# Kernel tuning notes

Hardware: AMD Instinct MI355X
Metric: run time of the kernel (lower is better)

## Reference

```python
import jax, jax.numpy as jnp
import numpy as np

B, N, DIM, HID, MAXN = 2048, 65536, 256, 512, 64
MID_KEY = (MAXN + HID) // 2   # 288
MID_VAL = (DIM + HID) // 2    # 384
MID_DEC = (HID + DIM) // 2    # 384
MID_SZ  = (HID + 1) // 2      # 256

def _ln(x, g, b):
    m = x.mean(-1, keepdims=True)
    v = ((x - m) ** 2).mean(-1, keepdims=True)
    return (x - m) * jax.lax.rsqrt(v + 1e-5) * g + b

def _mish(x):
    return x * jnp.tanh(jax.nn.softplus(x))

def _mlp_ln(x, W1, b1, g, be, W2, b2):
    return _mish(_ln(x @ W1 + b1, g, be)) @ W2 + b2

def _mlp(x, W1, b1, W2, b2):
    return _mish(x @ W1 + b1) @ W2 + b2

def setup_inputs():
    key = jax.random.key(0)
    ks = iter(jax.random.split(key, 40))
    def rn(shape, s=0.05):
        return jax.random.normal(next(ks), shape, jnp.float32) * s
    x = jax.random.normal(next(ks), (N, DIM), jnp.float32)
    batch = jnp.sort(jax.random.randint(next(ks), (N,), 0, B)).astype(jnp.int32)
    z32 = lambda *s: jnp.zeros(s, jnp.float32)
    o32 = lambda *s: jnp.ones(s, jnp.float32)
    return dict(
        x=x, batch=batch, n_batches=B,
        e_rank_W=rn((DIM, 1)), e_rank_b=z32(1),
        e_card_W=rn((1, HID)), e_card_b=z32(HID),
        e_key_W1=rn((MAXN, MID_KEY)), e_key_b1=z32(MID_KEY), e_key_g=o32(MID_KEY), e_key_be=z32(MID_KEY),
        e_key_W2=rn((MID_KEY, HID)), e_key_b2=z32(HID),
        e_val_W1=rn((DIM, MID_VAL)), e_val_b1=z32(MID_VAL), e_val_g=o32(MID_VAL), e_val_be=z32(MID_VAL),
        e_val_W2=rn((MID_VAL, HID)), e_val_b2=z32(HID),
        d_key_W1=rn((MAXN, MID_KEY)), d_key_b1=z32(MID_KEY), d_key_g=o32(MID_KEY), d_key_be=z32(MID_KEY),
        d_key_W2=rn((MID_KEY, HID)), d_key_b2=z32(HID),
        d_dec_W1=rn((HID, MID_DEC)), d_dec_b1=z32(MID_DEC),
        d_dec_W2=rn((MID_DEC, DIM)), d_dec_b2=z32(DIM),
        d_size_W1=rn((HID, MID_SZ)), d_size_b1=z32(MID_SZ), d_size_g=o32(MID_SZ), d_size_be=z32(MID_SZ),
        d_size_W2=rn((MID_SZ, 1)), d_size_b2=z32(1),
    )

def reference(x, batch, n_batches, e_rank_W, e_rank_b, e_card_W, e_card_b,
              e_key_W1, e_key_b1, e_key_g, e_key_be, e_key_W2, e_key_b2,
              e_val_W1, e_val_b1, e_val_g, e_val_be, e_val_W2, e_val_b2,
              d_key_W1, d_key_b1, d_key_g, d_key_be, d_key_W2, d_key_b2,
              d_dec_W1, d_dec_b1, d_dec_W2, d_dec_b2,
              d_size_W1, d_size_b1, d_size_g, d_size_be, d_size_W2, d_size_b2):
    max_n = e_key_W1.shape[0]
    n_pts = x.shape[0]
    # ---- Encoder ----
    n = jax.ops.segment_sum(jnp.ones(n_pts, jnp.float32), batch, num_segments=n_batches).astype(jnp.int32)
    mag = jnp.abs(x @ e_rank_W + e_rank_b)[:, 0]                 # [N]
    sort_key = batch.astype(jnp.float32) * jnp.max(mag) + mag    # sort within each set by |rank|
    idx = jnp.argsort(sort_key)
    xs = x[idx]
    starts = jnp.cumsum(n) - n                                   # per-set offsets (batch is sorted)
    pos_idx = jnp.arange(n_pts) - starts[batch]                  # rank within each set
    pos = jax.nn.one_hot(pos_idx, max_n, dtype=x.dtype)
    y = _mlp_ln(xs, e_val_W1, e_val_b1, e_val_g, e_val_be, e_val_W2, e_val_b2) \
      * _mlp_ln(pos, e_key_W1, e_key_b1, e_key_g, e_key_be, e_key_W2, e_key_b2)
    z = jax.ops.segment_sum(y, batch, num_segments=n_batches) \
      + n.astype(jnp.float32)[:, None] @ e_card_W + e_card_b     # [B, HID]
    # ---- Decoder ----
    n_logits = _mlp_ln(z, d_size_W1, d_size_b1, d_size_g, d_size_be, d_size_W2, d_size_b2)  # [B, 1]
    n_dec = jnp.clip(jnp.round(n_logits[:, 0]), 0, max_n).astype(jnp.int32)
    keys = _mlp_ln(jnp.eye(max_n, dtype=x.dtype),                # onehot positions 0..max_n-1
                   d_key_W1, d_key_b1, d_key_g, d_key_be, d_key_W2, d_key_b2)  # [max_n, HID]
    zp = z[:, None, :] * keys[None, :, :]                        # [B, max_n, HID] (repeat_interleave -> dense+mask)
    xf = _mlp(zp, d_dec_W1, d_dec_b1, d_dec_W2, d_dec_b2)        # [B, max_n, DIM]
    mask = jnp.arange(max_n)[None, :] < n_dec[:, None]           # valid rows per set
    x_out = (xf * mask[..., None].astype(xf.dtype)).reshape(-1, xf.shape[-1])
    batch_out = jnp.repeat(jnp.arange(n_batches, dtype=jnp.int32), max_n)
    return x_out, batch_out, mask.reshape(-1)
```

## Files before the change

kernel.cpp:

```cpp
#include <hip/hip_runtime.h>

#define NPTS   65536
#define NB     2048
#define DIMX   256
#define HIDN   512
#define MAXNN  64
#define MIDK   288
#define MIDV   384
#define MIDD   384
#define MIDS   256

typedef unsigned short ushort_t;
typedef __attribute__((ext_vector_type(8))) short short8;
typedef __attribute__((ext_vector_type(4))) float f32x4;

__device__ __forceinline__ float mishf(float x) {
    float e = __expf(fminf(x, 30.f));
    float n = e * (e + 2.f);
    return x * n * __builtin_amdgcn_rcpf(n + 2.f);
}
__device__ __forceinline__ ushort_t f2bf(float f) {
    unsigned u = __float_as_uint(f);
    u += 0x7fffu + ((u >> 16) & 1u);
    return (ushort_t)(u >> 16);
// ... 47 lines not shown
__global__ __launch_bounds__(256)
void k_rank(const int* __restrict__ batch, const float* __restrict__ mag,
            const unsigned int* __restrict__ maxmag, int* __restrict__ kidx)
{
    int i = blockIdx.x * 256 + threadIdx.x;
    if (i >= NPTS) return;
    int b = batch[i];
    int s = lbound(batch, 0, NPTS, b);
    int e = lbound(batch, s, NPTS, b + 1);
    float M = __uint_as_float(*maxmag);
    float kb = __fmul_rn((float)b, M);
    float ki = __fadd_rn(kb, mag[i]);
    int r = 0;
    for (int j = s; j < e; ++j) {
        float kj = __fadd_rn(kb, mag[j]);
        r += (kj < ki) || (kj == ki && j < i);
    }
    kidx[i] = (r < MAXNN) ? r : MAXNN;
}

__global__ __launch_bounds__(512)
void k_setup(const float* __restrict__ eW1, const float* __restrict__ eb1,
             const float* __restrict__ eg, const float* __restrict__ ebe,
             const float* __restrict__ eW2, const float* __restrict__ eb2,
             const float* __restrict__ dW1, const float* __restrict__ db1,
             const float* __restrict__ dg, const float* __restrict__ dbe,
             const float* __restrict__ dW2, const float* __restrict__ db2,
             float* __restrict__ enc_tbl, float* __restrict__ dec_tbl,
             const int* __restrict__ batch, const float* __restrict__ cardW,
             const float* __restrict__ cardb, float* __restrict__ z,
             const float* __restrict__ V0, ushort_t* __restrict__ T0,
             const float* __restrict__ V1, ushort_t* __restrict__ T1,
             const float* __restrict__ V2, ushort_t* __restrict__ T2,
             const float* __restrict__ V3, ushort_t* __restrict__ T3)
{
    const int blk = blockIdx.x;
    const int t = threadIdx.x;
    if (blk < 129) {
        const float *W1, *b1, *g, *be, *W2, *b2; float* out; int wrow;
        if (blk < 65) {
            W1 = eW1; b1 = eb1; g = eg; be = ebe; W2 = eW2; b2 = eb2;
            out = enc_tbl + blk * HIDN; wrow = (blk < 64) ? blk : -1;
        } else {
            int r = blk - 65;
            W1 = dW1; b1 = db1; g = dg; be = dbe; W2 = dW2; b2 = db2;
            out = dec_tbl + r * HIDN; wrow = r;
        }
        __shared__ float h[MIDK];
        __shared__ float red[512];
        float v = 0.f;
        if (t < MIDK) v = b1[t] + (wrow >= 0 ? W1[wrow * MIDK + t] : 0.f);
        red[t] = (t < MIDK) ? v : 0.f;
        __syncthreads();
        for (int o = 256; o > 0; o >>= 1) { if (t < o) red[t] += red[t + o]; __syncthreads(); }
        float m = red[0] / (float)MIDK;
        __syncthreads();
        float d = v - m;
        red[t] = (t < MIDK) ? d * d : 0.f;
        __syncthreads();
        for (int o = 256; o > 0; o >>= 1) { if (t < o) red[t] += red[t + o]; __syncthreads(); }
        float rs = rsqrtf(red[0] / (float)MIDK + 1e-5f);
        __syncthreads();
        if (t < MIDK) h[t] = mishf(d * rs * g[t] + be[t]);
        __syncthreads();
        float acc = b2[t];
        #pragma unroll 8
        for (int k = 0; k < MIDK; ++k) acc = fmaf(h[k], W2[k * HIDN + t], acc);
        out[t] = acc;
    } else if (blk < 129 + NB) {
        int b = blk - 129;
// ... 59 lines not shown
        if (t < o) {
            #pragma unroll
            for (int gI = 0; gI < 4; ++gI) red[gI][t] += red[gI][t + o];
        }
        __syncthreads();
    }
    float rs[4];
    #pragma unroll
    for (int gI = 0; gI < 4; ++gI) rs[gI] = rsqrtf(red[gI][0] * (1.f / 256.f) + 1e-5f);
    __syncthreads();
    float w2 = W2[t], gg = g[t], bbe = be[t];
    #pragma unroll
    for (int gI = 0; gI < 4; ++gI) {
        float h = mishf((acc[gI] - mm[gI]) * rs[gI] * gg + bbe);
        red[gI][t] = h * w2;
    }
    __syncthreads();
    for (int o = 128; o > 0; o >>= 1) {
        if (t < o) {
            #pragma unroll
            for (int gI = 0; gI < 4; ++gI) red[gI][t] += red[gI][t + o];
        }
        __syncthreads();
    }
    if (t < 4) {
        float logit = red[t][0] + b2[0];
        float n = rintf(logit);
        n = fminf(fmaxf(n, 0.f), 64.f);
        ndec[b0 + t] = (int)n;
    }
}

__global__ __launch_bounds__(256)
void k_compact_pad(const int* __restrict__ ndec, int* __restrict__ rowmap,
                   int* __restrict__ cntpad)
{
    __shared__ int lcnt;
    const int t = threadIdx.x;
    if (t == 0) lcnt = 0;
    __syncthreads();
    for (int b = t; b < NB; b += 256) {
        int n = ndec[b];
        if (n > 0) {
            int base = atomicAdd(&lcnt, n);
            for (int p = 0; p < n; ++p) rowmap[base + p] = b * 64 + p;
        }
    }
    __syncthreads();
    int c = lcnt;
    int pad = (c + 127) & ~127;
    for (int i = c + t; i < pad; i += 256) rowmap[i] = -1;
    if (t == 0) *cntpad = pad;
}

__global__ __launch_bounds__(256)
void k_tail(const int* __restrict__ ndec, float* __restrict__ outb,
            float* __restrict__ outm)
{
    int r = blockIdx.x * 256 + threadIdx.x;
    if (r < NB * MAXNN) {
        outb[r] = (float)(r >> 6);
        outm[r] = ((r & 63) < ndec[r >> 6]) ? 1.f : 0.f;
    }
}

__global__ __launch_bounds__(512, 2)
void k_enc(const ushort_t* __restrict__ A, const ushort_t* __restrict__ B1t,
           const float* __restrict__ b1, const float* __restrict__ g,
           const float* __restrict__ be, const ushort_t* __restrict__ B2t,
           const float* __restrict__ b2, const float* __restrict__ tbl,
           const int* __restrict__ kidx, const int* __restrict__ batch,
           float* __restrict__ zout)
{
    const int m0 = blockIdx.x * 128;
    __shared__ __align__(16) char SMEM[132096];
    ushort_t* slab = (ushort_t*)SMEM;
    ushort_t* As   = slab;
    ushort_t* Bs   = slab + 8192;
    ushort_t* Bs2  = (ushort_t*)(SMEM + 98304);
    float*    yred = (float*)(SMEM + 98304);
    float*    ssum = (float*)(SMEM + 98304);
    float*    ssq  = ssum + 512;
    int*      barr = (int*)(SMEM + 131072);
    int*      karr = barr + 128;

    const int t = threadIdx.x;
    const int l = t & 63;
    const int w = t >> 6;
    const int l4 = (l >> 4) << 2;
    const int drow = l >> 3;
    const int dblk = (l & 7) ^ drow;

    const int wmA = (w >> 2) * 64;
    const int wqA = (w & 3) * 96;
    f32x4 acc[4][6];
    #pragma unroll
    for (int a = 0; a < 4; ++a)
        #pragma unroll
        for (int b = 0; b < 6; ++b) acc[a][b] = (f32x4)0.f;

    for (int k0 = 0; k0 < DIMX; k0 += 64) {
        #pragma unroll
        for (int ii = 0; ii < 2; ++ii) {
            int i = w * 2 + ii;
            dma16(A + (size_t)(m0 + i * 8 + drow) * DIMX + k0 + dblk * 8, &As[i * 512]);
        }
        #pragma unroll
        for (int ii = 0; ii < 6; ++ii) {
            int i = w * 6 + ii;
            dma16(B1t + (size_t)(i * 8 + drow) * DIMX + k0 + dblk * 8, &Bs[i * 512]);
        }
        __syncthreads();
        #pragma unroll
        for (int ks = 0; ks < 2; ++ks) {
            int kq = ks * 4 + (l >> 4);
            short8 af[4], bfr[6];
            #pragma unroll
            for (int fm = 0; fm < 4; ++fm) {
                int row = wmA + fm * 16 + (l & 15);
                af[fm] = *(const short8*)&As[row * 64 + ((kq ^ (row & 7)) << 3)];
            }
            #pragma unroll
            for (int fn = 0; fn < 6; ++fn) {
                int row = wqA + fn * 16 + (l & 15);
                bfr[fn] = *(const short8*)&Bs[row * 64 + ((kq ^ (row & 7)) << 3)];
            }
            #pragma unroll
            for (int fm = 0; fm < 4; ++fm)
                #pragma unroll
                for (int fn = 0; fn < 6; ++fn)
                    acc[fm][fn] = __builtin_amdgcn_mfma_f32_16x16x32_bf16(
                        af[fm], bfr[fn], acc[fm][fn], 0, 0, 0);
        }
        __syncthreads();
    }

    float bb[6], gg[6], bee[6];
    #pragma unroll
    for (int fn = 0; fn < 6; ++fn) {
        int col = wqA + fn * 16 + (l & 15);
        bb[fn] = b1[col]; gg[fn] = g[col]; bee[fn] = be[col];
    }
    #pragma unroll
    for (int fm = 0; fm < 4; ++fm)
        #pragma unroll
        for (int fn = 0; fn < 6; ++fn)
            #pragma unroll
            for (int j = 0; j < 4; ++j) acc[fm][fn][j] += bb[fn];

    #pragma unroll
    for (int fm = 0; fm < 4; ++fm) {
        #pragma unroll
        for (int j = 0; j < 4; ++j) {
            float s = 0.f, q = 0.f;
            #pragma unroll
            for (int fn = 0; fn < 6; ++fn) {
                float v = acc[fm][fn][j];
                s += v; q += v * v;
            }
            #pragma unroll
            for (int o = 1; o < 16; o <<= 1) {
                s += __shfl_xor(s, o);
                q += __shfl_xor(q, o);
            }
            if ((l & 15) == 0) {
                int r = wmA + fm * 16 + l4 + j;
                ssum[r * 4 + (w & 3)] = s;
                ssq[r * 4 + (w & 3)] = q;
            }
        }
    }
    if (t < 128) { barr[t] = batch[m0 + t]; karr[t] = kidx[m0 + t]; }
    __syncthreads();

    #pragma unroll
    for (int fm = 0; fm < 4; ++fm) {
        #pragma unroll
        for (int j = 0; j < 4; ++j) {
            int r = wmA + fm * 16 + l4 + j;
            float s = ssum[r * 4 + 0] + ssum[r * 4 + 1] + ssum[r * 4 + 2] + ssum[r * 4 + 3];
            float q = ssq[r * 4 + 0] + ssq[r * 4 + 1] + ssq[r * 4 + 2] + ssq[r * 4 + 3];
            float m = s * (1.f / 384.f);
            float var = q * (1.f / 384.f) - m * m;
            float rs = rsqrtf(var + 1e-5f);
            #pragma unroll
            for (int fn = 0; fn < 6; ++fn) {
                float v = (acc[fm][fn][j] - m) * rs * gg[fn] + bee[fn];
                int c = wqA + fn * 16 + (l & 15);
                int panel = c >> 6, cc = c & 63;
                int kb = (cc >> 3) ^ (r & 7);
                slab[panel * 8192 + r * 64 + kb * 8 + (cc & 7)] = f2bf(mishf(v));
            }
        }
    }
    __syncthreads();

    const int wmB = (w >> 1) * 32;
    const int wnB = (w & 1) * 64;
    for (int nt = 0; nt < 4; ++nt) {
        const int n0t = nt * 128;
        f32x4 acc2[2][4];
        #pragma unroll
        for (int a = 0; a < 2; ++a)
            #pragma unroll
            for (int b = 0; b < 4; ++b) acc2[a][b] = (f32x4)0.f;

        for (int k0 = 0; k0 < MIDV; k0 += 128) {
            #pragma unroll
            for (int ii = 0; ii < 4; ++ii) {
                int pp = ii >> 1;
                int i = w * 2 + (ii & 1);
                dma16(B2t + (size_t)(n0t + i * 8 + drow) * MIDV + k0 + pp * 64 + dblk * 8,
                      &Bs2[pp * 8192 + i * 512]);
            }
            __syncthreads();
            #pragma unroll
            for (int ks = 0; ks < 4; ++ks) {
                int kq = ks * 4 + (l >> 4);
                int pp = kq >> 3, kb = kq & 7;
                int panel = (k0 >> 6) + pp;
                short8 af[2], bfr[4];
                #pragma unroll
                for (int fm = 0; fm < 2; ++fm) {
                    int row = wmB + fm * 16 + (l & 15);
                    af[fm] = *(const short8*)&slab[panel * 8192 + row * 64
                                                   + ((kb ^ (row & 7)) << 3)];
                }
                #pragma unroll
                for (int fn = 0; fn < 4; ++fn) {
                    int row = wnB + fn * 16 + (l & 15);
                    bfr[fn] = *(const short8*)&Bs2[pp * 8192 + row * 64
                                                   + ((kb ^ (row & 7)) << 3)];
                }
                #pragma unroll
                for (int fm = 0; fm < 2; ++fm)
                    #pragma unroll
                    for (int fn = 0; fn < 4; ++fn)
                        acc2[fm][fn] = __builtin_amdgcn_mfma_f32_16x16x32_bf16(
                            af[fm], bfr[fn], acc2[fm][fn], 0, 0, 0);
            }
            __syncthreads();
        }

        #pragma unroll
        for (int ph = 0; ph < 2; ++ph) {
            if ((w >> 2) == ph) {
                int rowbase = ((w >> 1) & 1) * 32;
                #pragma unroll
                for (int fn = 0; fn < 4; ++fn) {
                    int cl = wnB + fn * 16 + (l & 15);
                    float bbv = b2[n0t + cl];
                    #pragma unroll
                    for (int fm = 0; fm < 2; ++fm) {
                        #pragma unroll
                        for (int j = 0; j < 4; ++j) {
                            int rl = rowbase + fm * 16 + l4 + j;
                            int rg = ph * 64 + rl;
                            float v = (acc2[fm][fn][j] + bbv)
                                    * tbl[karr[rg] * HIDN + n0t + cl];
                            yred[cl * 64 + (rl ^ (cl & 31))] = v;
                        }
                    }
                }
            }
            __syncthreads();
            if (t < 256) {
                int c = t & 127, q = t >> 7;
                int gc = n0t + c;
                int base = q * 32;
                float run = 0.f; int curb = -1;
                #pragma unroll
                for (int ch = 0; ch < 2; ++ch) {
                    float v16[16]; int b16[16];
                    #pragma unroll
                    for (int rr = 0; rr < 16; ++rr) {
                        int rl = base + ch * 16 + rr;
                        v16[rr] = yred[c * 64 + (rl ^ (c & 31))];
                        b16[rr] = barr[ph * 64 + rl];
                    }
                    #pragma unroll
                    for (int rr = 0; rr < 16; ++rr) {
                        if (b16[rr] != curb) {
                            if (curb >= 0) atomicAdd(&zout[curb * HIDN + gc], run);
                            curb = b16[rr]; run = v16[rr];
                        } else run += v16[rr];
                    }
                }
                atomicAdd(&zout[curb * HIDN + gc], run);
            }
            __syncthreads();
        }
    }
}

template<int MODE>
__device__ __forceinline__
void mm_body(const ushort_t* __restrict__ A, const ushort_t* __restrict__ Bt,
             const float* __restrict__ bias, void* __restrict__ Cptr, int K,
             const float* __restrict__ tbl, const float* __restrict__ zin,
             const int* __restrict__ rowmap, const int* __restrict__ cntpad)
{
    const int flat = blockIdx.y * gridDim.x + blockIdx.x;
    const int nx = gridDim.x;
    const int xcd = flat & 7;
    const int lin = flat >> 3;
    const int n0 = (lin % nx) * 128;
    const int m0 = ((lin / nx) + ((gridDim.y >> 3) * xcd)) * 128;
    if (m0 >= *cntpad) return;
    __shared__ __align__(16) ushort_t sAB[2 * 128 * 64];
    ushort_t* As = sAB;
    ushort_t* Bs = sAB + 128 * 64;
    const int t = threadIdx.x;
    const int l = t & 63;
    const int w = t >> 6;
    const int wm = (w >> 1) * 64;
    const int wn = (w & 1) * 64;
    const int l4 = (l >> 4) << 2;
    const int drow = l >> 3;
    const int dblk = (l & 7) ^ drow;

    int g4[4], p4[4];
    if (MODE == 2) {
        #pragma unroll
        for (int ii = 0; ii < 4; ++ii) {
// ... 138 lines not shown
    const float* e_val_b2 = (const float*)d_in[18];
    const float* d_key_W1 = (const float*)d_in[19];
    const float* d_key_b1 = (const float*)d_in[20];
    const float* d_key_g  = (const float*)d_in[21];
    const float* d_key_be = (const float*)d_in[22];
    const float* d_key_W2 = (const float*)d_in[23];
    const float* d_key_b2 = (const float*)d_in[24];
    const float* d_dec_W1 = (const float*)d_in[25];
    const float* d_dec_b1 = (const float*)d_in[26];
    const float* d_dec_W2 = (const float*)d_in[27];
    const float* d_dec_b2 = (const float*)d_in[28];
    const float* d_size_W1= (const float*)d_in[29];
    const float* d_size_b1= (const float*)d_in[30];
    const float* d_size_g = (const float*)d_in[31];
    const float* d_size_be= (const float*)d_in[32];
    const float* d_size_W2= (const float*)d_in[33];
    const float* d_size_b2= (const float*)d_in[34];

    char* ws = (char*)d_ws;
    unsigned int* maxmag  = (unsigned int*)(ws + 8448);
    int*          kidx    = (int*)         (ws + 8704);
    float*        mag     = (float*)       (ws + 270848);
    float*        enc_tbl = (float*)       (ws + 532992);
    float*        dec_tbl = (float*)       (ws + 666112);
    float*        z       = (float*)       (ws + 797184);
    int*          ndec    = (int*)         (ws + 4991488);
    int*          cntpad  = (int*)         (ws + 4999684);
    int*          rowmap  = (int*)         (ws + 5000192);
    ushort_t*     evW1t   = (ushort_t*)    (ws + 5524480);
    ushort_t*     evW2t   = (ushort_t*)    (ws + 5721088);
    ushort_t*     ddW1t   = (ushort_t*)    (ws + 6114304);
    ushort_t*     ddW2t   = (ushort_t*)    (ws + 6507520);
    ushort_t*     xb      = (ushort_t*)    (ws + 6704384);
    ushort_t*     Hd      = (ushort_t*)    (ws + 6704384 + 33554432);

    float* out_x = (float*)d_out;
    float* out_b = out_x + (size_t)NB * MAXNN * DIMX;
    float* out_m = out_b + NB * MAXNN;

    hipMemsetAsync(out_x, 0, (size_t)NB * MAXNN * DIMX * sizeof(float), stream);
    hipMemsetAsync(maxmag, 0, 4, stream);
    k_mag<<<dim3(4096), dim3(256), 0, stream>>>(x, e_rank_W, e_rank_b, mag, maxmag, xb);
    k_rank<<<dim3(256), dim3(256), 0, stream>>>(batch, mag, maxmag, kidx);
    k_setup<<<dim3(129 + NB + 1152), dim3(512), 0, stream>>>(
        e_key_W1, e_key_b1, e_key_g, e_key_be, e_key_W2, e_key_b2,
        d_key_W1, d_key_b1, d_key_g, d_key_be, d_key_W2, d_key_b2,
        enc_tbl, dec_tbl, batch, e_card_W, e_card_b, z,
        e_val_W1, evW1t, e_val_W2, evW2t, d_dec_W1, ddW1t, d_dec_W2, ddW2t);

    k_enc<<<dim3(512), dim3(512), 0, stream>>>(xb, evW1t, e_val_b1, e_val_g, e_val_be,
                                               evW2t, e_val_b2, enc_tbl, kidx, batch, z);

    k_size<<<dim3(NB / 4), dim3(256), 0, stream>>>(z, d_size_W1, d_size_b1, d_size_g,
                                                   d_size_be, d_size_W2, d_size_b2, ndec);
    k_compact_pad<<<dim3(1), dim3(256), 0, stream>>>(ndec, rowmap, cntpad);
    k_mm_d1<<<dim3(3, 1024), dim3(256), 0, stream>>>(ddW1t, d_dec_b1, Hd, HIDN,
                                                     dec_tbl, z, rowmap, cntpad);
    k_mm_d2<<<dim3(2, 1024), dim3(256), 0, stream>>>(Hd, ddW2t, d_dec_b2, out_x, MIDD,
                                                     rowmap, cntpad);
    k_tail<<<dim3(512), dim3(256), 0, stream>>>(ndec, out_b, out_m);
}
```

Before: 505.5 us.

## Halve encoder tile height, fuse output zeroing and tail into post kernel

The encoder kernel now handles 64 rows per block instead of 128 and runs on 1024 blocks. It uses smaller shared-memory staging (about 80KB), streams B1 in two halves, and raises launch bounds to 4 blocks per CU to improve occupancy. The two memsets are removed: maxmag is zeroed inside k_setup, and out_x is zeroed together with the batch/mask tail and the rowmap compaction in a single k_post kernel. k_mag and k_rank are reordered to run after k_setup. The trade-off is more B-matrix reloads per row and more atomics into z from the smaller tiles, and the per-kernel register budget is tighter.

New measurement: 508.6 us. No clear change (+0.6%).

```diff
diff --git a/kernel.cpp b/kernel.cpp
--- a/kernel.cpp
+++ b/kernel.cpp
@@ -103,10 +103,12 @@
              const float* __restrict__ V0, ushort_t* __restrict__ T0,
              const float* __restrict__ V1, ushort_t* __restrict__ T1,
              const float* __restrict__ V2, ushort_t* __restrict__ T2,
-             const float* __restrict__ V3, ushort_t* __restrict__ T3)
+             const float* __restrict__ V3, ushort_t* __restrict__ T3,
+             unsigned int* __restrict__ maxmag)
 {
     const int blk = blockIdx.x;
     const int t = threadIdx.x;
+    if (blk == 0 && t == 0) *maxmag = 0u;
     if (blk < 129) {
         const float *W1, *b1, *g, *be, *W2, *b2; float* out; int wrow;
         if (blk < 65) {
@@ -232,39 +234,39 @@
 }
 
 __global__ __launch_bounds__(256)
-void k_compact_pad(const int* __restrict__ ndec, int* __restrict__ rowmap,
-                   int* __restrict__ cntpad)
+void k_post(const int* __restrict__ ndec, float* __restrict__ out_x,
+            float* __restrict__ outb, float* __restrict__ outm,
+            int* __restrict__ rowmap, int* __restrict__ cntpad)
 {
-    __shared__ int lcnt;
-    const int t = threadIdx.x;
-    if (t == 0) lcnt = 0;
-    __syncthreads();
-    for (int b = t; b < NB; b += 256) {
-        int n = ndec[b];
-        if (n > 0) {
-            int base = atomicAdd(&lcnt, n);
-            for (int p = 0; p < n; ++p) rowmap[base + p] = b * 64 + p;
-        }
-    }
-    __syncthreads();
-    int c = lcnt;
-    int pad = (c + 127) & ~127;
-    for (int i = c + t; i < pad; i += 256) rowmap[i] = -1;
-    if (t == 0) *cntpad = pad;
-}
-
-__global__ __launch_bounds__(256)
-void k_tail(const int* __restrict__ ndec, float* __restrict__ outb,
-            float* __restrict__ outm)
-{
-    int r = blockIdx.x * 256 + threadIdx.x;
-    if (r < NB * MAXNN) {
-        outb[r] = (float)(r >> 6);
-        outm[r] = ((r & 63) < ndec[r >> 6]) ? 1.f : 0.f;
-    }
-}
-
-__global__ __launch_bounds__(512, 2)
+    const int gidx = blockIdx.x * 256 + threadIdx.x;
+    float4 z4 = make_float4(0.f, 0.f, 0.f, 0.f);
+    float4* p = (float4*)out_x;
+    #pragma unroll
+    for (int i = 0; i < 32; ++i) p[gidx + i * 262144] = z4;
+    if (gidx < NB * MAXNN) {
+        outb[gidx] = (float)(gidx >> 6);
+        outm[gidx] = ((gidx & 63) < ndec[gidx >> 6]) ? 1.f : 0.f;
+    }
+    if (blockIdx.x == 0) {
+        __shared__ int lcnt;
+        if (threadIdx.x == 0) lcnt = 0;
+        __syncthreads();
+        for (int b = threadIdx.x; b < NB; b += 256) {
+            int n = ndec[b];
+            if (n > 0) {
+                int base = atomicAdd(&lcnt, n);
+                for (int q = 0; q < n; ++q) rowmap[base + q] = b * 64 + q;
+            }
+        }
+        __syncthreads();
+        int c = lcnt;
+        int pad = (c + 127) & ~127;
+        for (int i = c + threadIdx.x; i < pad; i += 256) rowmap[i] = -1;
+        if (threadIdx.x == 0) *cntpad = pad;
+    }
+}
+
+__global__ __launch_bounds__(512, 4)
 void k_enc(const ushort_t* __restrict__ A, const ushort_t* __restrict__ B1t,
            const float* __restrict__ b1, const float* __restrict__ g,
            const float* __restrict__ be, const ushort_t* __restrict__ B2t,
@@ -272,17 +274,15 @@
            const int* __restrict__ kidx, const int* __restrict__ batch,
            float* __restrict__ zout)
 {
-    const int m0 = blockIdx.x * 128;
-    __shared__ __align__(16) char SMEM[132096];
+    const int m0 = blockIdx.x * 64;
+    __shared__ __align__(16) char SMEM[81920];
     ushort_t* slab = (ushort_t*)SMEM;
-    ushort_t* As   = slab;
-    ushort_t* Bs   = slab + 8192;
-    ushort_t* Bs2  = (ushort_t*)(SMEM + 98304);
-    float*    yred = (float*)(SMEM + 98304);
-    float*    ssum = (float*)(SMEM + 98304);
-    float*    ssq  = ssum + 512;
-    int*      barr = (int*)(SMEM + 131072);
-    int*      karr = barr + 128;
+    ushort_t* As   = (ushort_t*)(SMEM + 49152);
+    ushort_t* Bs   = (ushort_t*)(SMEM + 57344);
+    ushort_t* Bs2  = (ushort_t*)(SMEM + 49152);
+    float*    yred = (float*)(SMEM + 49152);
+    float*    ssum = (float*)(SMEM + 49152);
+    float*    ssq  = ssum + 256;
 
     const int t = threadIdx.x;
     const int l = t & 63;
@@ -291,71 +291,71 @@
     const int drow = l >> 3;
     const int dblk = (l & 7) ^ drow;
 
-    const int wmA = (w >> 2) * 64;
-    const int wqA = (w & 3) * 96;
-    f32x4 acc[4][6];
-    #pragma unroll
-    for (int a = 0; a < 4; ++a)
+    const int wr = w >> 2;
+    const int wc = w & 3;
+    f32x4 acc[2][6];
+    #pragma unroll
+    for (int a = 0; a < 2; ++a)
         #pragma unroll
         for (int b = 0; b < 6; ++b) acc[a][b] = (f32x4)0.f;
 
     for (int k0 = 0; k0 < DIMX; k0 += 64) {
-        #pragma unroll
-        for (int ii = 0; ii < 2; ++ii) {
-            int i = w * 2 + ii;
-            dma16(A + (size_t)(m0 + i * 8 + drow) * DIMX + k0 + dblk * 8, &As[i * 512]);
-        }
-        #pragma unroll
-        for (int ii = 0; ii < 6; ++ii) {
-            int i = w * 6 + ii;
-            dma16(B1t + (size_t)(i * 8 + drow) * DIMX + k0 + dblk * 8, &Bs[i * 512]);
-        }
-        __syncthreads();
-        #pragma unroll
-        for (int ks = 0; ks < 2; ++ks) {
-            int kq = ks * 4 + (l >> 4);
-            short8 af[4], bfr[6];
-            #pragma unroll
-            for (int fm = 0; fm < 4; ++fm) {
-                int row = wmA + fm * 16 + (l & 15);
-                af[fm] = *(const short8*)&As[row * 64 + ((kq ^ (row & 7)) << 3)];
-            }
-            #pragma unroll
-            for (int fn = 0; fn < 6; ++fn) {
-                int row = wqA + fn * 16 + (l & 15);
-                bfr[fn] = *(const short8*)&Bs[row * 64 + ((kq ^ (row & 7)) << 3)];
-            }
-            #pragma unroll
-            for (int fm = 0; fm < 4; ++fm)
-                #pragma unroll
-                for (int fn = 0; fn < 6; ++fn)
-                    acc[fm][fn] = __builtin_amdgcn_mfma_f32_16x16x32_bf16(
-                        af[fm], bfr[fn], acc[fm][fn], 0, 0, 0);
-        }
-        __syncthreads();
+        dma16(A + (size_t)(m0 + w * 8 + drow) * DIMX + k0 + dblk * 8, As + w * 512);
+        #pragma unroll
+        for (int h = 0; h < 2; ++h) {
+            #pragma unroll
+            for (int ii = 0; ii < 3; ++ii) {
+                int rloc = w * 24 + ii * 8;
+                dma16(B1t + (size_t)(h * 192 + rloc + drow) * DIMX + k0 + dblk * 8,
+                      Bs + rloc * 64);
+            }
+            __syncthreads();
+            #pragma unroll
+            for (int ks = 0; ks < 2; ++ks) {
+                int kq = ks * 4 + (l >> 4);
+                short8 af[2], bf3[3];
+                #pragma unroll
+                for (int fm = 0; fm < 2; ++fm) {
+                    int row = wr * 32 + fm * 16 + (l & 15);
+                    af[fm] = *(const short8*)&As[row * 64 + ((kq ^ (row & 7)) << 3)];
+                }
+                #pragma unroll
+                for (int cf = 0; cf < 3; ++cf) {
+                    int rloc = wc * 48 + cf * 16 + (l & 15);
+                    bf3[cf] = *(const short8*)&Bs[rloc * 64 + ((kq ^ (rloc & 7)) << 3)];
+                }
+                #pragma unroll
+                for (int fm = 0; fm < 2; ++fm)
+                    #pragma unroll
+                    for (int cf = 0; cf < 3; ++cf)
+                        acc[fm][h * 3 + cf] = __builtin_amdgcn_mfma_f32_16x16x32_bf16(
+                            af[fm], bf3[cf], acc[fm][h * 3 + cf], 0, 0, 0);
+            }
+            __syncthreads();
+        }
     }
 
     float bb[6], gg[6], bee[6];
     #pragma unroll
-    for (int fn = 0; fn < 6; ++fn) {
-        int col = wqA + fn * 16 + (l & 15);
-        bb[fn] = b1[col]; gg[fn] = g[col]; bee[fn] = be[col];
-    }
-    #pragma unroll
-    for (int fm = 0; fm < 4; ++fm)
-        #pragma unroll
-        for (int fn = 0; fn < 6; ++fn)
-            #pragma unroll
-            for (int j = 0; j < 4; ++j) acc[fm][fn][j] += bb[fn];
-
-    #pragma unroll
-    for (int fm = 0; fm < 4; ++fm) {
+    for (int fc = 0; fc < 6; ++fc) {
+        int col = (fc / 3) * 192 + wc * 48 + (fc % 3) * 16 + (l & 15);
+        bb[fc] = b1[col]; gg[fc] = g[col]; bee[fc] = be[col];
+    }
+    #pragma unroll
+    for (int fm = 0; fm < 2; ++fm)
+        #pragma unroll
+        for (int fc = 0; fc < 6; ++fc)
+            #pragma unroll
+            for (int j = 0; j < 4; ++j) acc[fm][fc][j] += bb[fc];
+
+    #pragma unroll
+    for (int fm = 0; fm < 2; ++fm) {
         #pragma unroll
         for (int j = 0; j < 4; ++j) {
             float s = 0.f, q = 0.f;
             #pragma unroll
-            for (int fn = 0; fn < 6; ++fn) {
-                float v = acc[fm][fn][j];
+            for (int fc = 0; fc < 6; ++fc) {
+                float v = acc[fm][fc][j];
                 s += v; q += v * v;
             }
             #pragma unroll
@@ -364,132 +364,127 @@
                 q += __shfl_xor(q, o);
             }
             if ((l & 15) == 0) {
-                int r = wmA + fm * 16 + l4 + j;
-                ssum[r * 4 + (w & 3)] = s;
-                ssq[r * 4 + (w & 3)] = q;
-            }
-        }
-    }
-    if (t < 128) { barr[t] = batch[m0 + t]; karr[t] = kidx[m0 + t]; }
-    __syncthreads();
-
-    #pragma unroll
-    for (int fm = 0; fm < 4; ++fm) {
+                int r = wr * 32 + fm * 16 + l4 + j;
+                ssum[r * 4 + wc] = s;
+                ssq[r * 4 + wc] = q;
+            }
+        }
+    }
+    __syncthreads();
+
+    #pragma unroll
+    for (int fm = 0; fm < 2; ++fm) {
         #pragma unroll
         for (int j = 0; j < 4; ++j) {
-            int r = wmA + fm * 16 + l4 + j;
+            int r = wr * 32 + fm * 16 + l4 + j;
             float s = ssum[r * 4 + 0] + ssum[r * 4 + 1] + ssum[r * 4 + 2] + ssum[r * 4 + 3];
             float q = ssq[r * 4 + 0] + ssq[r * 4 + 1] + ssq[r * 4 + 2] + ssq[r * 4 + 3];
             float m = s * (1.f / 384.f);
             float var = q * (1.f / 384.f) - m * m;
             float rs = rsqrtf(var + 1e-5f);
             #pragma unroll
-            for (int fn = 0; fn < 6; ++fn) {
-                float v = (acc[fm][fn][j] - m) * rs * gg[fn] + bee[fn];
-                int c = wqA + fn * 16 + (l & 15);
+            for (int fc = 0; fc < 6; ++fc) {
+                float v = (acc[fm][fc][j] - m) * rs * gg[fc] + bee[fc];
+                int c = (fc / 3) * 192 + wc * 48 + (fc % 3) * 16 + (l & 15);
                 int panel = c >> 6, cc = c & 63;
                 int kb = (cc >> 3) ^ (r & 7);
-                slab[panel * 8192 + r * 64 + kb * 8 + (cc & 7)] = f2bf(mishf(v));
-            }
-        }
-    }
-    __syncthreads();
-
-    const int wmB = (w >> 1) * 32;
-    const int wnB = (w & 1) * 64;
+                slab[panel * 4096 + r * 64 + kb * 8 + (cc & 7)] = f2bf(mishf(v));
+            }
+        }
+    }
+    __syncthreads();
+
+    const int wr2 = w >> 2;
+    const int wc2 = w & 3;
+    int kid8[2][4];
+    #pragma unroll
+    for (int fm = 0; fm < 2; ++fm)
+        #pragma unroll
+        for (int j = 0; j < 4; ++j)
+            kid8[fm][j] = kidx[m0 + wr2 * 32 + fm * 16 + l4 + j];
+
     for (int nt = 0; nt < 4; ++nt) {
         const int n0t = nt * 128;
-        f32x4 acc2[2][4];
+        f32x4 acc2[2][2];
         #pragma unroll
         for (int a = 0; a < 2; ++a)
             #pragma unroll
-            for (int b = 0; b < 4; ++b) acc2[a][b] = (f32x4)0.f;
-
-        for (int k0 = 0; k0 < MIDV; k0 += 128) {
-            #pragma unroll
-            for (int ii = 0; ii < 4; ++ii) {
-                int pp = ii >> 1;
-                int i = w * 2 + (ii & 1);
-                dma16(B2t + (size_t)(n0t + i * 8 + drow) * MIDV + k0 + pp * 64 + dblk * 8,
-                      &Bs2[pp * 8192 + i * 512]);
+            for (int b = 0; b < 2; ++b) acc2[a][b] = (f32x4)0.f;
+
+        for (int k0 = 0; k0 < MIDV; k0 += 64) {
+            #pragma unroll
+            for (int ii = 0; ii < 2; ++ii) {
+                int nr = w * 16 + ii * 8;
+                dma16(B2t + (size_t)(n0t + nr + drow) * MIDV + k0 + dblk * 8,
+                      Bs2 + nr * 64);
             }
             __syncthreads();
-            #pragma unroll
-            for (int ks = 0; ks < 4; ++ks) {
+            const int panel = k0 >> 6;
+            #pragma unroll
+            for (int ks = 0; ks < 2; ++ks) {
                 int kq = ks * 4 + (l >> 4);
-                int pp = kq >> 3, kb = kq & 7;
-                int panel = (k0 >> 6) + pp;
-                short8 af[2], bfr[4];
+                short8 af[2], bf2v[2];
                 #pragma unroll
                 for (int fm = 0; fm < 2; ++fm) {
-                    int row = wmB + fm * 16 + (l & 15);
-                    af[fm] = *(const short8*)&slab[panel * 8192 + row * 64
-                                                   + ((kb ^ (row & 7)) << 3)];
+                    int row = wr2 * 32 + fm * 16 + (l & 15);
+                    af[fm] = *(const short8*)&slab[panel * 4096 + row * 64
+                                                   + ((kq ^ (row & 7)) << 3)];
                 }
                 #pragma unroll
-                for (int fn = 0; fn < 4; ++fn) {
-                    int row = wnB + fn * 16 + (l & 15);
-                    bfr[fn] = *(const short8*)&Bs2[pp * 8192 + row * 64
-                                                   + ((kb ^ (row & 7)) << 3)];
+                for (int fn = 0; fn < 2; ++fn) {
+                    int nr = wc2 * 32 + fn * 16 + (l & 15);
+                    bf2v[fn] = *(const short8*)&Bs2[nr * 64 + ((kq ^ (nr & 7)) << 3)];
                 }
                 #pragma unroll
                 for (int fm = 0; fm < 2; ++fm)
                     #pragma unroll
-                    for (int fn = 0; fn < 4; ++fn)
+                    for (int fn = 0; fn < 2; ++fn)
                         acc2[fm][fn] = __builtin_amdgcn_mfma_f32_16x16x32_bf16(
-                            af[fm], bfr[fn], acc2[fm][fn], 0, 0, 0);
+                            af[fm], bf2v[fn], acc2[fm][fn], 0, 0, 0);
             }
             __syncthreads();
         }
 
         #pragma unroll
-        for (int ph = 0; ph < 2; ++ph) {
-            if ((w >> 2) == ph) {
-                int rowbase = ((w >> 1) & 1) * 32;
-                #pragma unroll
-                for (int fn = 0; fn < 4; ++fn) {
-                    int cl = wnB + fn * 16 + (l & 15);
-                    float bbv = b2[n0t + cl];
-                    #pragma unroll
-                    for (int fm = 0; fm < 2; ++fm) {
-                        #pragma unroll
-                        for (int j = 0; j < 4; ++j) {
-                            int rl = rowbase + fm * 16 + l4 + j;
-                            int rg = ph * 64 + rl;
-                            float v = (acc2[fm][fn][j] + bbv)
-                                    * tbl[karr[rg] * HIDN + n0t + cl];
-                            yred[cl * 64 + (rl ^ (cl & 31))] = v;
-                        }
-                    }
+        for (int fn = 0; fn < 2; ++fn) {
+            int cl = wc2 * 32 + fn * 16 + (l & 15);
+            float bbv = b2[n0t + cl];
+            #pragma unroll
+            for (int fm = 0; fm < 2; ++fm) {
+                #pragma unroll
+                for (int j = 0; j < 4; ++j) {
+                    int rl = wr2 * 32 + fm * 16 + l4 + j;
+                    float v = (acc2[fm][fn][j] + bbv)
+                            * tbl[kid8[fm][j] * HIDN + n0t + cl];
+                    yred[cl * 64 + (rl ^ (cl & 31))] = v;
                 }
             }
-            __syncthreads();
-            if (t < 256) {
-                int c = t & 127, q = t >> 7;
-                int gc = n0t + c;
-                int base = q * 32;
-                float run = 0.f; int curb = -1;
-                #pragma unroll
-                for (int ch = 0; ch < 2; ++ch) {
-                    float v16[16]; int b16[16];
-                    #pragma unroll
-                    for (int rr = 0; rr < 16; ++rr) {
-                        int rl = base + ch * 16 + rr;
-                        v16[rr] = yred[c * 64 + (rl ^ (c & 31))];
-                        b16[rr] = barr[ph * 64 + rl];
-                    }
-                    #pragma unroll
-                    for (int rr = 0; rr < 16; ++rr) {
-                        if (b16[rr] != curb) {
-                            if (curb >= 0) atomicAdd(&zout[curb * HIDN + gc], run);
-                            curb = b16[rr]; run = v16[rr];
-                        } else run += v16[rr];
-                    }
+        }
+        __syncthreads();
+        if (t < 256) {
+            int c = t & 127, q = t >> 7;
+            int gc = n0t + c;
+            float run = 0.f; int curb = -1;
+            #pragma unroll
+            for (int ch = 0; ch < 2; ++ch) {
+                float v16[16]; int b16[16];
+                #pragma unroll
+                for (int rr = 0; rr < 16; ++rr) {
+                    int rl = q * 32 + ch * 16 + rr;
+                    v16[rr] = yred[c * 64 + (rl ^ (c & 31))];
+                    b16[rr] = batch[m0 + rl];
                 }
-                atomicAdd(&zout[curb * HIDN + gc], run);
-            }
-            __syncthreads();
-        }
+                #pragma unroll
+                for (int rr = 0; rr < 16; ++rr) {
+                    if (b16[rr] != curb) {
+                        if (curb >= 0) atomicAdd(&zout[curb * HIDN + gc], run);
+                        curb = b16[rr]; run = v16[rr];
+                    } else run += v16[rr];
+                }
+            }
+            atomicAdd(&zout[curb * HIDN + gc], run);
+        }
+        __syncthreads();
     }
 }
 
@@ -700,25 +695,24 @@
     float* out_b = out_x + (size_t)NB * MAXNN * DIMX;
     float* out_m = out_b + NB * MAXNN;
 
-    hipMemsetAsync(out_x, 0, (size_t)NB * MAXNN * DIMX * sizeof(float), stream);
-    hipMemsetAsync(maxmag, 0, 4, stream);
-    k_mag<<<dim3(4096), dim3(256), 0, stream>>>(x, e_rank_W, e_rank_b, mag, maxmag, xb);
-    k_rank<<<dim3(256), dim3(256), 0, stream>>>(batch, mag, maxmag, kidx);
     k_setup<<<dim3(129 + NB + 1152), dim3(512), 0, stream>>>(
         e_key_W1, e_key_b1, e_key_g, e_key_be, e_key_W2, e_key_b2,
         d_key_W1, d_key_b1, d_key_g, d_key_be, d_key_W2, d_key_b2,
         enc_tbl, dec_tbl, batch, e_card_W, e_card_b, z,
-        e_val_W1, evW1t, e_val_W2, evW2t, d_dec_W1, ddW1t, d_dec_W2, ddW2t);
-
-    k_enc<<<dim3(512), dim3(512), 0, stream>>>(xb, evW1t, e_val_b1, e_val_g, e_val_be,
-                                               evW2t, e_val_b2, enc_tbl, kidx, batch, z);
+        e_val_W1, evW1t, e_val_W2, evW2t, d_dec_W1, ddW1t, d_dec_W2, ddW2t,
+        maxmag);
+    k_mag<<<dim3(4096), dim3(256), 0, stream>>>(x, e_rank_W, e_rank_b, mag, maxmag, xb);
+    k_rank<<<dim3(256), dim3(256), 0, stream>>>(batch, mag, maxmag, kidx);
+
+    k_enc<<<dim3(1024), dim3(512), 0, stream>>>(xb, evW1t, e_val_b1, e_val_g, e_val_be,
+                                                evW2t, e_val_b2, enc_tbl, kidx, batch, z);
 
     k_size<<<dim3(NB / 4), dim3(256), 0, stream>>>(z, d_size_W1, d_size_b1, d_size_g,
                                                    d_size_be, d_size_W2, d_size_b2, ndec);
-    k_compact_pad<<<dim3(1), dim3(256), 0, stream>>>(ndec, rowmap, cntpad);
+    k_post<<<dim3(1024), dim3(256), 0, stream>>>(ndec, out_x, out_b, out_m,
+                                                 rowmap, cntpad);
     k_mm_d1<<<dim3(3, 1024), dim3(256), 0, stream>>>(ddW1t, d_dec_b1, Hd, HIDN,
                                                      dec_tbl, z, rowmap, cntpad);
     k_mm_d2<<<dim3(2, 1024), dim3(256), 0, stream>>>(Hd, ddW2t, d_dec_b2, out_x, MIDD,
                                                      rowmap, cntpad);
-    k_tail<<<dim3(512), dim3(256), 0, stream>>>(ndec, out_b, out_m);
-}
+}
```

## Split fused encoder into two GEMM kernels and merge post-processing kernels

Applied to the files above, without the earlier changes.

The single fused encoder kernel, which computed both MLP layers per 128-row tile with a large LDS footprint, is split into two kernels. The first-layer kernel writes a bf16 hidden buffer to global memory, and a separate 4x512-grid GEMM does the second layer with the segment-sum epilogue. This aims to raise occupancy and parallelism at the cost of an extra global round trip of the hidden activations. The output memset, tail and compaction kernels are merged into one k_post kernel, and the maxmag reset moves into k_setup to cut launch and memset overhead.

After: 484.6 us. 1.04x faster.

```diff
diff --git a/kernel.cpp b/kernel.cpp
--- a/kernel.cpp
+++ b/kernel.cpp
@@ -103,10 +103,12 @@
              const float* __restrict__ V0, ushort_t* __restrict__ T0,
              const float* __restrict__ V1, ushort_t* __restrict__ T1,
              const float* __restrict__ V2, ushort_t* __restrict__ T2,
-             const float* __restrict__ V3, ushort_t* __restrict__ T3)
+             const float* __restrict__ V3, ushort_t* __restrict__ T3,
+             unsigned int* __restrict__ maxmag)
 {
     const int blk = blockIdx.x;
     const int t = threadIdx.x;
+    if (blk == 0 && t == 0) *maxmag = 0u;
     if (blk < 129) {
         const float *W1, *b1, *g, *be, *W2, *b2; float* out; int wrow;
         if (blk < 65) {
@@ -232,67 +234,55 @@
 }
 
 __global__ __launch_bounds__(256)
-void k_compact_pad(const int* __restrict__ ndec, int* __restrict__ rowmap,
-                   int* __restrict__ cntpad)
-{
-    __shared__ int lcnt;
-    const int t = threadIdx.x;
-    if (t == 0) lcnt = 0;
-    __syncthreads();
-    for (int b = t; b < NB; b += 256) {
-        int n = ndec[b];
-        if (n > 0) {
-            int base = atomicAdd(&lcnt, n);
-            for (int p = 0; p < n; ++p) rowmap[base + p] = b * 64 + p;
-        }
-    }
-    __syncthreads();
-    int c = lcnt;
-    int pad = (c + 127) & ~127;
-    for (int i = c + t; i < pad; i += 256) rowmap[i] = -1;
-    if (t == 0) *cntpad = pad;
-}
-
-__global__ __launch_bounds__(256)
-void k_tail(const int* __restrict__ ndec, float* __restrict__ outb,
-            float* __restrict__ outm)
-{
-    int r = blockIdx.x * 256 + threadIdx.x;
-    if (r < NB * MAXNN) {
-        outb[r] = (float)(r >> 6);
-        outm[r] = ((r & 63) < ndec[r >> 6]) ? 1.f : 0.f;
+void k_post(const int* __restrict__ ndec, float* __restrict__ out_x,
+            float* __restrict__ outb, float* __restrict__ outm,
+            int* __restrict__ rowmap, int* __restrict__ cntpad)
+{
+    const int gidx = blockIdx.x * 256 + threadIdx.x;
+    float4 z4 = make_float4(0.f, 0.f, 0.f, 0.f);
+    float4* p = (float4*)out_x;
+    #pragma unroll
+    for (int i = 0; i < 32; ++i) p[gidx + i * 262144] = z4;
+    if (gidx < NB * MAXNN) {
+        outb[gidx] = (float)(gidx >> 6);
+        outm[gidx] = ((gidx & 63) < ndec[gidx >> 6]) ? 1.f : 0.f;
+    }
+    if (blockIdx.x == 0) {
+        __shared__ int lcnt;
+        if (threadIdx.x == 0) lcnt = 0;
+        __syncthreads();
+        for (int b = threadIdx.x; b < NB; b += 256) {
+            int n = ndec[b];
+            if (n > 0) {
+                int base = atomicAdd(&lcnt, n);
+                for (int q = 0; q < n; ++q) rowmap[base + q] = b * 64 + q;
+            }
+        }
+        __syncthreads();
+        int c = lcnt;
+        int pad = (c + 127) & ~127;
+        for (int i = c + threadIdx.x; i < pad; i += 256) rowmap[i] = -1;
+        if (threadIdx.x == 0) *cntpad = pad;
     }
 }
 
 __global__ __launch_bounds__(512, 2)
-void k_enc(const ushort_t* __restrict__ A, const ushort_t* __restrict__ B1t,
-           const float* __restrict__ b1, const float* __restrict__ g,
-           const float* __restrict__ be, const ushort_t* __restrict__ B2t,
-           const float* __restrict__ b2, const float* __restrict__ tbl,
-           const int* __restrict__ kidx, const int* __restrict__ batch,
-           float* __restrict__ zout)
+void k_mm_e1f(const ushort_t* __restrict__ A, const ushort_t* __restrict__ Bt,
+              const float* __restrict__ bias, const float* __restrict__ g,
+              const float* __restrict__ be, ushort_t* __restrict__ C)
 {
     const int m0 = blockIdx.x * 128;
-    __shared__ __align__(16) char SMEM[132096];
-    ushort_t* slab = (ushort_t*)SMEM;
-    ushort_t* As   = slab;
-    ushort_t* Bs   = slab + 8192;
-    ushort_t* Bs2  = (ushort_t*)(SMEM + 98304);
-    float*    yred = (float*)(SMEM + 98304);
-    float*    ssum = (float*)(SMEM + 98304);
-    float*    ssq  = ssum + 512;
-    int*      barr = (int*)(SMEM + 131072);
-    int*      karr = barr + 128;
-
+    __shared__ __align__(16) ushort_t As[128 * 64];
+    __shared__ __align__(16) ushort_t Bs[384 * 64];
     const int t = threadIdx.x;
     const int l = t & 63;
     const int w = t >> 6;
+    const int wm = (w >> 2) * 64;
+    const int wq = (w & 3) * 96;
     const int l4 = (l >> 4) << 2;
     const int drow = l >> 3;
     const int dblk = (l & 7) ^ drow;
 
-    const int wmA = (w >> 2) * 64;
-    const int wqA = (w & 3) * 96;
     f32x4 acc[4][6];
     #pragma unroll
     for (int a = 0; a < 4; ++a)
@@ -308,7 +298,7 @@
         #pragma unroll
         for (int ii = 0; ii < 6; ++ii) {
             int i = w * 6 + ii;
-            dma16(B1t + (size_t)(i * 8 + drow) * DIMX + k0 + dblk * 8, &Bs[i * 512]);
+            dma16(Bt + (size_t)(i * 8 + drow) * DIMX + k0 + dblk * 8, &Bs[i * 512]);
         }
         __syncthreads();
         #pragma unroll
@@ -317,12 +307,12 @@
             short8 af[4], bfr[6];
             #pragma unroll
             for (int fm = 0; fm < 4; ++fm) {
-                int row = wmA + fm * 16 + (l & 15);
+                int row = wm + fm * 16 + (l & 15);
                 af[fm] = *(const short8*)&As[row * 64 + ((kq ^ (row & 7)) << 3)];
             }
             #pragma unroll
             for (int fn = 0; fn < 6; ++fn) {
-                int row = wqA + fn * 16 + (l & 15);
+                int row = wq + fn * 16 + (l & 15);
                 bfr[fn] = *(const short8*)&Bs[row * 64 + ((kq ^ (row & 7)) << 3)];
             }
             #pragma unroll
@@ -338,8 +328,8 @@
     float bb[6], gg[6], bee[6];
     #pragma unroll
     for (int fn = 0; fn < 6; ++fn) {
-        int col = wqA + fn * 16 + (l & 15);
-        bb[fn] = b1[col]; gg[fn] = g[col]; bee[fn] = be[col];
+        int col = wq + fn * 16 + (l & 15);
+        bb[fn] = bias[col]; gg[fn] = g[col]; bee[fn] = be[col];
     }
     #pragma unroll
     for (int fm = 0; fm < 4; ++fm)
@@ -348,6 +338,8 @@
             #pragma unroll
             for (int j = 0; j < 4; ++j) acc[fm][fn][j] += bb[fn];
 
+    float* ssum = (float*)As;
+    float* ssq  = ssum + 512;
     #pragma unroll
     for (int fm = 0; fm < 4; ++fm) {
         #pragma unroll
@@ -364,20 +356,18 @@
                 q += __shfl_xor(q, o);
             }
             if ((l & 15) == 0) {
-                int r = wmA + fm * 16 + l4 + j;
+                int r = wm + fm * 16 + l4 + j;
                 ssum[r * 4 + (w & 3)] = s;
                 ssq[r * 4 + (w & 3)] = q;
             }
         }
     }
-    if (t < 128) { barr[t] = batch[m0 + t]; karr[t] = kidx[m0 + t]; }
     __syncthreads();
-
     #pragma unroll
     for (int fm = 0; fm < 4; ++fm) {
         #pragma unroll
         for (int j = 0; j < 4; ++j) {
-            int r = wmA + fm * 16 + l4 + j;
+            int r = wm + fm * 16 + l4 + j;
             float s = ssum[r * 4 + 0] + ssum[r * 4 + 1] + ssum[r * 4 + 2] + ssum[r * 4 + 3];
             float q = ssq[r * 4 + 0] + ssq[r * 4 + 1] + ssq[r * 4 + 2] + ssq[r * 4 + 3];
             float m = s * (1.f / 384.f);
@@ -386,110 +376,127 @@
             #pragma unroll
             for (int fn = 0; fn < 6; ++fn) {
                 float v = (acc[fm][fn][j] - m) * rs * gg[fn] + bee[fn];
-                int c = wqA + fn * 16 + (l & 15);
-                int panel = c >> 6, cc = c & 63;
-                int kb = (cc >> 3) ^ (r & 7);
-                slab[panel * 8192 + r * 64 + kb * 8 + (cc & 7)] = f2bf(mishf(v));
-            }
-        }
-    }
-    __syncthreads();
-
-    const int wmB = (w >> 1) * 32;
-    const int wnB = (w & 1) * 64;
-    for (int nt = 0; nt < 4; ++nt) {
-        const int n0t = nt * 128;
-        f32x4 acc2[2][4];
-        #pragma unroll
-        for (int a = 0; a < 2; ++a)
-            #pragma unroll
-            for (int b = 0; b < 4; ++b) acc2[a][b] = (f32x4)0.f;
-
-        for (int k0 = 0; k0 < MIDV; k0 += 128) {
-            #pragma unroll
-            for (int ii = 0; ii < 4; ++ii) {
-                int pp = ii >> 1;
-                int i = w * 2 + (ii & 1);
-                dma16(B2t + (size_t)(n0t + i * 8 + drow) * MIDV + k0 + pp * 64 + dblk * 8,
-                      &Bs2[pp * 8192 + i * 512]);
-            }
-            __syncthreads();
-            #pragma unroll
-            for (int ks = 0; ks < 4; ++ks) {
-                int kq = ks * 4 + (l >> 4);
-                int pp = kq >> 3, kb = kq & 7;
-                int panel = (k0 >> 6) + pp;
-                short8 af[2], bfr[4];
+                C[(size_t)(m0 + r) * MIDV + wq + fn * 16 + (l & 15)] = f2bf(mishf(v));
+            }
+        }
+    }
+}
+
+__global__ __launch_bounds__(256, 2)
+void k_mm_e2(const ushort_t* __restrict__ A, const ushort_t* __restrict__ Bt,
+             const float* __restrict__ bias, int K, const float* __restrict__ tbl,
+             const int* __restrict__ kidx, const int* __restrict__ batch,
+             float* __restrict__ zout)
+{
+    const int flat = blockIdx.y * gridDim.x + blockIdx.x;
+    const int nx = gridDim.x;
+    const int xcd = flat & 7;
+    const int lin = flat >> 3;
+    const int n0 = (lin % nx) * 128;
+    const int m0 = ((lin / nx) + ((gridDim.y >> 3) * xcd)) * 128;
+    __shared__ __align__(16) ushort_t sAB[2 * 128 * 64];
+    __shared__ int barr[128];
+    __shared__ int karr[128];
+    ushort_t* As = sAB;
+    ushort_t* Bs = sAB + 128 * 64;
+    const int t = threadIdx.x;
+    const int l = t & 63;
+    const int w = t >> 6;
+    const int wm = (w >> 1) * 64;
+    const int wn = (w & 1) * 64;
+    const int l4 = (l >> 4) << 2;
+    const int drow = l >> 3;
+    const int dblk = (l & 7) ^ drow;
+
+    if (t < 128) { barr[t] = batch[m0 + t]; karr[t] = kidx[m0 + t]; }
+
+    f32x4 acc[4][4];
+    #pragma unroll
+    for (int a = 0; a < 4; ++a)
+        #pragma unroll
+        for (int b = 0; b < 4; ++b) acc[a][b] = (f32x4)0.f;
+
+    for (int k0 = 0; k0 < K; k0 += 64) {
+        #pragma unroll
+        for (int ii = 0; ii < 4; ++ii) {
+            int i = w * 4 + ii;
+            dma16(A + (size_t)(m0 + i * 8 + drow) * K + k0 + dblk * 8, &As[i * 512]);
+        }
+        #pragma unroll
+        for (int ii = 0; ii < 4; ++ii) {
+            int i = w * 4 + ii;
+            dma16(Bt + (size_t)(n0 + i * 8 + drow) * K + k0 + dblk * 8, &Bs[i * 512]);
+        }
+        __syncthreads();
+        #pragma unroll
+        for (int ks = 0; ks < 2; ++ks) {
+            short8 af[4], bfr[4];
+            int kq = ks * 4 + (l >> 4);
+            #pragma unroll
+            for (int fm = 0; fm < 4; ++fm) {
+                int row = wm + fm * 16 + (l & 15);
+                af[fm] = *(const short8*)&As[row * 64 + ((kq ^ (row & 7)) << 3)];
+            }
+            #pragma unroll
+            for (int fn = 0; fn < 4; ++fn) {
+                int row = wn + fn * 16 + (l & 15);
+                bfr[fn] = *(const short8*)&Bs[row * 64 + ((kq ^ (row & 7)) << 3)];
+            }
+            #pragma unroll
+            for (int fm = 0; fm < 4; ++fm)
                 #pragma unroll
-                for (int fm = 0; fm < 2; ++fm) {
-                    int row = wmB + fm * 16 + (l & 15);
-                    af[fm] = *(const short8*)&slab[panel * 8192 + row * 64
-                                                   + ((kb ^ (row & 7)) << 3)];
+                for (int fn = 0; fn < 4; ++fn)
+                    acc[fm][fn] = __builtin_amdgcn_mfma_f32_16x16x32_bf16(
+                        af[fm], bfr[fn], acc[fm][fn], 0, 0, 0);
+        }
+        __syncthreads();
+    }
+
+    float* yred = (float*)sAB;
+    #pragma unroll
+    for (int pass = 0; pass < 2; ++pass) {
+        if ((w >> 1) == pass) {
+            #pragma unroll
+            for (int fn = 0; fn < 4; ++fn) {
+                int cl = wn + fn * 16 + (l & 15);
+                float bbv = bias[n0 + cl];
+                #pragma unroll
+                for (int fm = 0; fm < 4; ++fm) {
+                    #pragma unroll
+                    for (int j = 0; j < 4; ++j) {
+                        int rl = fm * 16 + l4 + j;
+                        float v = (acc[fm][fn][j] + bbv)
+                                * tbl[karr[pass * 64 + rl] * HIDN + (n0 + cl)];
+                        yred[cl * 64 + (rl ^ (cl & 31))] = v;
+                    }
+                }
+            }
+        }
+        __syncthreads();
+        {
+            int c = t & 127, q = t >> 7;
+            int gc = n0 + c;
+            float run = 0.f; int curb = -1;
+            #pragma unroll
+            for (int ch = 0; ch < 2; ++ch) {
+                float v16[16]; int b16[16];
+                #pragma unroll
+                for (int rr = 0; rr < 16; ++rr) {
+                    int rl = q * 32 + ch * 16 + rr;
+                    v16[rr] = yred[c * 64 + (rl ^ (c & 31))];
+                    b16[rr] = barr[pass * 64 + rl];
                 }
                 #pragma unroll
-                for (int fn = 0; fn < 4; ++fn) {
-                    int row = wnB + fn * 16 + (l & 15);
-                    bfr[fn] = *(const short8*)&Bs2[pp * 8192 + row * 64
-                                                   + ((kb ^ (row & 7)) << 3)];
+                for (int rr = 0; rr < 16; ++rr) {
+                    if (b16[rr] != curb) {
+                        if (curb >= 0) atomicAdd(&zout[curb * HIDN + gc], run);
+                        curb = b16[rr]; run = v16[rr];
+                    } else run += v16[rr];
                 }
-                #pragma unroll
-                for (int fm = 0; fm < 2; ++fm)
-                    #pragma unroll
-                    for (int fn = 0; fn < 4; ++fn)
-                        acc2[fm][fn] = __builtin_amdgcn_mfma_f32_16x16x32_bf16(
-                            af[fm], bfr[fn], acc2[fm][fn], 0, 0, 0);
-            }
-            __syncthreads();
-        }
-
-        #pragma unroll
-        for (int ph = 0; ph < 2; ++ph) {
-            if ((w >> 2) == ph) {
-                int rowbase = ((w >> 1) & 1) * 32;
-                #pragma unroll
-                for (int fn = 0; fn < 4; ++fn) {
-                    int cl = wnB + fn * 16 + (l & 15);
-                    float bbv = b2[n0t + cl];
-                    #pragma unroll
-                    for (int fm = 0; fm < 2; ++fm) {
-                        #pragma unroll
-                        for (int j = 0; j < 4; ++j) {
-                            int rl = rowbase + fm * 16 + l4 + j;
-                            int rg = ph * 64 + rl;
-                            float v = (acc2[fm][fn][j] + bbv)
-                                    * tbl[karr[rg] * HIDN + n0t + cl];
-                            yred[cl * 64 + (rl ^ (cl & 31))] = v;
-                        }
-                    }
-                }
-            }
-            __syncthreads();
-            if (t < 256) {
-                int c = t & 127, q = t >> 7;
-                int gc = n0t + c;
-                int base = q * 32;
-                float run = 0.f; int curb = -1;
-                #pragma unroll
-                for (int ch = 0; ch < 2; ++ch) {
-                    float v16[16]; int b16[16];
-                    #pragma unroll
-                    for (int rr = 0; rr < 16; ++rr) {
-                        int rl = base + ch * 16 + rr;
-                        v16[rr] = yred[c * 64 + (rl ^ (c & 31))];
-                        b16[rr] = barr[ph * 64 + rl];
-                    }
-                    #pragma unroll
-                    for (int rr = 0; rr < 16; ++rr) {
-                        if (b16[rr] != curb) {
-                            if (curb >= 0) atomicAdd(&zout[curb * HIDN + gc], run);
-                            curb = b16[rr]; run = v16[rr];
-                        } else run += v16[rr];
-                    }
-                }
-                atomicAdd(&zout[curb * HIDN + gc], run);
-            }
-            __syncthreads();
-        }
+            }
+            atomicAdd(&zout[curb * HIDN + gc], run);
+        }
+        __syncthreads();
     }
 }
 
@@ -694,31 +701,33 @@
     ushort_t*     ddW1t   = (ushort_t*)    (ws + 6114304);
     ushort_t*     ddW2t   = (ushort_t*)    (ws + 6507520);
     ushort_t*     xb      = (ushort_t*)    (ws + 6704384);
+    ushort_t*     Hb      = (ushort_t*)    (ws + 6704384 + 33554432);
     ushort_t*     Hd      = (ushort_t*)    (ws + 6704384 + 33554432);
 
     float* out_x = (float*)d_out;
     float* out_b = out_x + (size_t)NB * MAXNN * DIMX;
     float* out_m = out_b + NB * MAXNN;
 
-    hipMemsetAsync(out_x, 0, (size_t)NB * MAXNN * DIMX * sizeof(float), stream);
-    hipMemsetAsync(maxmag, 0, 4, stream);
-    k_mag<<<dim3(4096), dim3(256), 0, stream>>>(x, e_rank_W, e_rank_b, mag, maxmag, xb);
-    k_rank<<<dim3(256), dim3(256), 0, stream>>>(batch, mag, maxmag, kidx);
     k_setup<<<dim3(129 + NB + 1152), dim3(512), 0, stream>>>(
         e_key_W1, e_key_b1, e_key_g, e_key_be, e_key_W2, e_key_b2,
         d_key_W1, d_key_b1, d_key_g, d_key_be, d_key_W2, d_key_b2,
         enc_tbl, dec_tbl, batch, e_card_W, e_card_b, z,
-        e_val_W1, evW1t, e_val_W2, evW2t, d_dec_W1, ddW1t, d_dec_W2, ddW2t);
-
-    k_enc<<<dim3(512), dim3(512), 0, stream>>>(xb, evW1t, e_val_b1, e_val_g, e_val_be,
-                                               evW2t, e_val_b2, enc_tbl, kidx, batch, z);
+        e_val_W1, evW1t, e_val_W2, evW2t, d_dec_W1, ddW1t, d_dec_W2, ddW2t,
+        maxmag);
+    k_mag<<<dim3(4096), dim3(256), 0, stream>>>(x, e_rank_W, e_rank_b, mag, maxmag, xb);
+    k_rank<<<dim3(256), dim3(256), 0, stream>>>(batch, mag, maxmag, kidx);
+
+    k_mm_e1f<<<dim3(512), dim3(512), 0, stream>>>(xb, evW1t, e_val_b1,
+                                                  e_val_g, e_val_be, Hb);
+    k_mm_e2<<<dim3(4, 512), dim3(256), 0, stream>>>(Hb, evW2t, e_val_b2, MIDV,
+                                                    enc_tbl, kidx, batch, z);
 
     k_size<<<dim3(NB / 4), dim3(256), 0, stream>>>(z, d_size_W1, d_size_b1, d_size_g,
                                                    d_size_be, d_size_W2, d_size_b2, ndec);
-    k_compact_pad<<<dim3(1), dim3(256), 0, stream>>>(ndec, rowmap, cntpad);
+    k_post<<<dim3(1024), dim3(256), 0, stream>>>(ndec, out_x, out_b, out_m,
+                                                 rowmap, cntpad);
     k_mm_d1<<<dim3(3, 1024), dim3(256), 0, stream>>>(ddW1t, d_dec_b1, Hd, HIDN,
                                                      dec_tbl, z, rowmap, cntpad);
     k_mm_d2<<<dim3(2, 1024), dim3(256), 0, stream>>>(Hd, ddW2t, d_dec_b2, out_x, MIDD,
                                                      rowmap, cntpad);
-    k_tail<<<dim3(512), dim3(256), 0, stream>>>(ndec, out_b, out_m);
-}
+}
```
